# Kernel tuning notes

Measured on AMD Instinct MI355X. Metric: run time of the kernel, lower is better.

Reference implementation:

```python
import jax, jax.numpy as jnp
import numpy as np

DIM = 128
NUM_HEADS = 4
HEAD_DIM = DIM // NUM_HEADS
WS = 8            # window height/width
SHIFT = 4
N_CAND = 4        # candidates per spatial position
H_RES, W_RES = 64, 128
M = WS * WS       # tokens per window spatially
L = M * N_CAND    # window sequence length
NW = (H_RES // WS) * (W_RES // WS)
B = 1
B_ = NW * B
NEG_INF = -1e9  # finite stand-in for -inf; softmax result identical within fp tolerance


def _rel_position_index():
    ch = np.arange(WS); cw = np.arange(WS)
    coords = np.stack(np.meshgrid(ch, cw, indexing='ij')).reshape(2, -1)  # [2, M]
    rel = (coords[:, :, None] - coords[:, None, :]).transpose(1, 2, 0)    # [M, M, 2]
    rel = rel + np.array([WS - 1, WS - 1])
    rel[..., 0] *= 2 * WS - 1
    return rel.sum(-1).astype(np.int32)  # [M, M] in [0, (2WS-1)^2)


def _window_attn_mask():
    # block message passing between same spatial position's candidates (except self)
    idx = np.repeat(np.arange(M), N_CAND).astype(np.float64)  # [L]
    m = idx[:, None] - idx[None, :]
    mask = np.where(m == 0, NEG_INF, 0.0)
    mask[np.arange(L), np.arange(L)] = 0.0
    return mask  # [L, L]


def _shift_window_attn_mask():
    img = np.zeros((H_RES, W_RES))
    cnt = 0
    for hs in (slice(0, -WS), slice(-WS, -SHIFT), slice(-SHIFT, None)):
        for ws in (slice(0, -WS), slice(-WS, -SHIFT), slice(-SHIFT, None)):
            img[hs, ws] = cnt
            cnt += 1
    mw = img.reshape(H_RES // WS, WS, W_RES // WS, WS).transpose(0, 2, 1, 3).reshape(-1, M)  # [nW, M]
    am = mw[:, None, :] - mw[:, :, None]           # [nW, M, M]
    am = np.where(am != 0, NEG_INF, 0.0)
    am = np.repeat(np.repeat(am, N_CAND, axis=1), N_CAND, axis=2)  # [nW, L, L]
    return am + _window_attn_mask()[None]


def setup_inputs() -> dict:
    key = jax.random.key(0)
    ks = jax.random.split(key, 6)
    x = jax.random.normal(ks[0], (B_, L, DIM), dtype=jnp.float32)
    qkv_w = jax.random.normal(ks[1], (3 * DIM, DIM), dtype=jnp.float32) * 0.02
    qkv_b = jnp.zeros((3 * DIM,), dtype=jnp.float32)
    rpe_table = jax.random.normal(ks[2], ((2 * WS - 1) ** 2, 3 * DIM), dtype=jnp.float32) * 0.02
    proj_w = jax.random.normal(ks[3], (DIM, DIM), dtype=jnp.float32) * 0.02
    proj_b = jnp.zeros((DIM,), dtype=jnp.float32)
    attn_mask = jnp.asarray(_shift_window_attn_mask(), dtype=jnp.float32)
    rel_idx = jnp.asarray(_rel_position_index())
    return {"x": x, "qkv_w": qkv_w, "qkv_b": qkv_b, "rpe_table": rpe_table,
            "proj_w": proj_w, "proj_b": proj_b, "attn_mask": attn_mask, "rel_idx": rel_idx}


def reference(x, qkv_w, qkv_b, rpe_table, proj_w, proj_b, attn_mask, rel_idx):
    b_, l, _ = x.shape
    h, hd = NUM_HEADS, HEAD_DIM
    scale = hd ** -0.5
    # QKV projection -> [B_, h, L, hd] each
    qkv = (x @ qkv_w.T + qkv_b).reshape(b_, l, 3, h, hd).transpose(2, 0, 3, 1, 4)
    q, k, v = qkv[0], qkv[1], qkv[2]
    # relative-position encodings gathered per (i, j) pair, expanded over candidates
    m = rel_idx.shape[0]
    n = l // m
    rpe = rpe_table[rel_idx.reshape(-1)].reshape(m, m, h, 3 * hd)
    rpe = jnp.repeat(jnp.repeat(rpe, n, axis=0), n, axis=1)  # [L, L, h, 3*hd]
    q_rpe, k_rpe, v_rpe = jnp.split(rpe, 3, axis=-1)
    q = q * scale
    q_rpe = q_rpe * scale
    qk = jnp.einsum('bhic,bhjc->bhij', q, k)
    qr = jnp.einsum('bhic,ijhc->bhij', q, k_rpe)
    kr = jnp.einsum('bhjc,ijhc->bhij', k, q_rpe)
    attn = qk + qr + kr  # [B_, h, L, L]
    nw = attn_mask.shape[0]
    attn = attn.reshape(b_ // nw, nw, h, l, l) + attn_mask[None, :, None]
    attn = attn.reshape(b_, h, l, l)
    attn = jax.nn.softmax(attn.astype(jnp.float32), axis=-1).astype(x.dtype)
    out = jnp.einsum('bhij,bhjc->bhic', attn, v) + jnp.einsum('bhij,ijhc->bhic', attn, v_rpe)
    out = out.transpose(0, 2, 1, 3).reshape(b_, l, DIM)
    return out @ proj_w.T + proj_b
```

## Files before the change

### kernel.cpp

```cpp
#include <hip/hip_runtime.h>
#include <math.h>

constexpr int HD    = 32;
constexpr int LW    = 256;
constexpr int NWIN  = 128;
constexpr int ROWS  = NWIN * LW;
constexpr int QKVC  = 384;
constexpr float SCALE = 0.17677669529663687f;

__device__ inline float dot4(const float4 a, const float4 b) {
  return a.x * b.x + a.y * b.y + a.z * b.z + a.w * b.w;
}

__global__ __launch_bounds__(256) void rpe_gather_kernel(
    const float* __restrict__ tab, const int* __restrict__ rel_idx,
    float* __restrict__ out)
{
  int gid = blockIdx.x * 256 + threadIdx.x;
  int s   = gid % 96;
  int hp  = gid / 96;
  int p   = hp & 4095;
  int h   = hp >> 12;
  float v = tab[(size_t)rel_idx[p] * 384 + h * 96 + s];
  if (s < 32) v *= SCALE;
  out[gid] = v;
}

template <int N, int K>
__global__ __launch_bounds__(256) void gemm_nt_bias_v3(
    const float* __restrict__ A, const float* __restrict__ W,
    const float* __restrict__ bias, float* __restrict__ C)
{
  constexpr int BK  = 8;
  constexpr int NS  = K / BK;
  constexpr int LDP = 144;
  __shared__ float As[2][BK][LDP];
  __shared__ float Ws[2][BK][LDP];

  const int tid  = threadIdx.x;
  const int tx   = tid & 15;
  const int ty   = tid >> 4;
  const int srow = tid >> 1;
  const int skk  = (tid & 1) << 2;
  const int sphys = srow + ((srow >> 5) << 2);

  const float* Ag = A + ((size_t)blockIdx.x * 128 + srow) * K + skk;
  const float* Wg = W + ((size_t)blockIdx.y * 128 + srow) * K + skk;

  float4 ra = *(const float4*)(Ag);
  float4 rw = *(const float4*)(Wg);
  As[0][skk + 0][sphys] = ra.x; As[0][skk + 1][sphys] = ra.y;
  As[0][skk + 2][sphys] = ra.z; As[0][skk + 3][sphys] = ra.w;
  Ws[0][skk + 0][sphys] = rw.x; Ws[0][skk + 1][sphys] = rw.y;
  Ws[0][skk + 2][sphys] = rw.z; Ws[0][skk + 3][sphys] = rw.w;
  __syncthreads();

  const int mA = ty * 8; const int pA = mA + ((mA >> 5) << 2);
  const int mB = tx * 8; const int pB = mB + ((mB >> 5) << 2);

  float acc[8][8] = {};

  for (int s = 0; s < NS; ++s) {
    const int cur = s & 1;
    if (s + 1 < NS) {
      const int k0 = (s + 1) * BK;
      ra = *(const float4*)(Ag + k0);
      rw = *(const float4*)(Wg + k0);
    }
#pragma unroll
    for (int k = 0; k < BK; ++k) {
      float4 a0 = *(const float4*)&As[cur][k][pA];
      float4 a1 = *(const float4*)&As[cur][k][pA + 4];
      float4 b0 = *(const float4*)&Ws[cur][k][pB];
      float4 b1 = *(const float4*)&Ws[cur][k][pB + 4];
      float av[8] = {a0.x, a0.y, a0.z, a0.w, a1.x, a1.y, a1.z, a1.w};
      float bv[8] = {b0.x, b0.y, b0.z, b0.w, b1.x, b1.y, b1.z, b1.w};
#pragma unroll
      for (int i = 0; i < 8; ++i)
#pragma unroll
        for (int j = 0; j < 8; ++j)
          acc[i][j] += av[i] * bv[j];
    }
    if (s + 1 < NS) {
      const int nxt = (s + 1) & 1;
      As[nxt][skk + 0][sphys] = ra.x; As[nxt][skk + 1][sphys] = ra.y;
      As[nxt][skk + 2][sphys] = ra.z; As[nxt][skk + 3][sphys] = ra.w;
      Ws[nxt][skk + 0][sphys] = rw.x; Ws[nxt][skk + 1][sphys] = rw.y;
      Ws[nxt][skk + 2][sphys] = rw.z; Ws[nxt][skk + 3][sphys] = rw.w;
      __syncthreads();
    }
  }

  const int crow = blockIdx.x * 128 + ty * 8;
  const int ccol = blockIdx.y * 128 + tx * 8;
  float4 bb0 = *(const float4*)(bias + ccol);
  float4 bb1 = *(const float4*)(bias + ccol + 4);
#pragma unroll
  for (int i = 0; i < 8; ++i) {
    float4 r0, r1;
    r0.x = acc[i][0] + bb0.x; r0.y = acc[i][1] + bb0.y;
    r0.z = acc[i][2] + bb0.z; r0.w = acc[i][3] + bb0.w;
    r1.x = acc[i][4] + bb1.x; r1.y = acc[i][5] + bb1.y;
    r1.z = acc[i][6] + bb1.z; r1.w = acc[i][7] + bb1.w;
    *(float4*)(C + (size_t)(crow + i) * N + ccol)     = r0;
    *(float4*)(C + (size_t)(crow + i) * N + ccol + 4) = r1;
  }
}

__global__ __launch_bounds__(512) void attn_kernel(
    const float* __restrict__ qkv, const float* __restrict__ rpeg,
    const float* __restrict__ mask, float* __restrict__ out)
{
  __shared__ float ms[256 * 33];
  const int b = blockIdx.x;
  const int h = blockIdx.y;
  const int tid = threadIdx.x;
  const int row = tid & 255;
  const int jh  = __builtin_amdgcn_readfirstlane(tid >> 8);
  const size_t rowbase = (size_t)b * LW;

  const float* kvbase = qkv + rowbase * QKVC + 128 + h * HD;

  float4 q[8];
  {
    const float4* qr = (const float4*)(qkv + (rowbase + row) * QKVC + h * HD);
#pragma unroll
    for (int d = 0; d < 8; ++d) {
      float4 t = qr[d];
      q[d] = make_float4(t.x * SCALE, t.y * SCALE, t.z * SCALE, t.w * SCALE);
    }
  }
  const float4* rp4base =
      (const float4*)(rpeg + ((size_t)h * 4096 + (size_t)(row >> 2) * 64) * 96);
  const float* mrow = mask + ((size_t)b * LW + row) * LW;

  float4 acc[8];
#pragma unroll
  for (int d = 0; d < 8; ++d) acc[d] = make_float4(0.f, 0.f, 0.f, 0.f);
  float l_run = 0.f;
  const int jbase = jh << 5;

  for (int l = 0; l < 32; ++l) {
    const int j4 = jbase + l;
    const float4* rp = rp4base + j4 * 24;
    float4 uq[8];
    float c0 = 0.f;
#pragma unroll
    for (int d = 0; d < 8; ++d) {
      float4 sq = rp[d];
      float4 kr = rp[8 + d];
      uq[d] = make_float4(q[d].x + sq.x, q[d].y + sq.y,
                          q[d].z + sq.z, q[d].w + sq.w);
      c0 += dot4(q[d], kr);
    }
    float4 mv = *(const float4*)(mrow + j4 * 4);
    const float* kj0 = kvbase + (size_t)(j4 * 4) * QKVC;
    float s[4] = {mv.x + c0, mv.y + c0, mv.z + c0, mv.w + c0};
#pragma unroll
    for (int jc = 0; jc < 4; ++jc) {
      const float4* kj = (const float4*)(kj0 + jc * QKVC);
      float sa = 0.f;
#pragma unroll
      for (int d = 0; d < 8; ++d) sa += dot4(uq[d], kj[d]);
      s[jc] += sa;
    }
    float p[4];
    p[0] = __expf(s[0]); p[1] = __expf(s[1]);
    p[2] = __expf(s[2]); p[3] = __expf(s[3]);
    float pool = (p[0] + p[1]) + (p[2] + p[3]);
    l_run += pool;
#pragma unroll
    for (int jc = 0; jc < 4; ++jc) {
      const float4* vj = (const float4*)(kj0 + jc * QKVC + 128);
      float pj = p[jc];
#pragma unroll
      for (int d = 0; d < 8; ++d) {
        acc[d].x += pj * vj[d].x; acc[d].y += pj * vj[d].y;
        acc[d].z += pj * vj[d].z; acc[d].w += pj * vj[d].w;
      }
    }
#pragma unroll
    for (int d = 0; d < 8; ++d) {
      float4 vr = rp[16 + d];
      acc[d].x += pool * vr.x; acc[d].y += pool * vr.y;
      acc[d].z += pool * vr.z; acc[d].w += pool * vr.w;
    }
  }

  __syncthreads();
  if (jh == 1) {
    float* dst = &ms[row * 33];
#pragma unroll
    for (int d = 0; d < 8; ++d) {
      dst[d * 4 + 0] = acc[d].x; dst[d * 4 + 1] = acc[d].y;
      dst[d * 4 + 2] = acc[d].z; dst[d * 4 + 3] = acc[d].w;
    }
    dst[32] = l_run;
  }
  __syncthreads();
  if (jh == 0) {
    const float* src = &ms[row * 33];
    float inv = 1.f / (l_run + src[32]);
    float4* orow = (float4*)(out + (rowbase + row) * (4 * HD) + h * HD);
#pragma unroll
    for (int d = 0; d < 8; ++d) {
      float4 r;
      r.x = (acc[d].x + src[d * 4 + 0]) * inv;
      r.y = (acc[d].y + src[d * 4 + 1]) * inv;
      r.z = (acc[d].z + src[d * 4 + 2]) * inv;
      r.w = (acc[d].w + src[d * 4 + 3]) * inv;
      orow[d] = r;
    }
  }
}

extern "C" void kernel_launch(void* const* d_in, const int* in_sizes, int n_in,
                              void* d_out, int out_size, void* d_ws, size_t ws_size,
                              hipStream_t stream) {
  (void)in_sizes; (void)n_in; (void)out_size; (void)ws_size;
  const float* x         = (const float*)d_in[0];
  const float* qkv_w     = (const float*)d_in[1];
  const float* qkv_b     = (const float*)d_in[2];
  const float* rpe_table = (const float*)d_in[3];
  const float* proj_w    = (const float*)d_in[4];
  const float* proj_b    = (const float*)d_in[5];
  const float* attn_mask = (const float*)d_in[6];
  const int*   rel_idx   = (const int*)d_in[7];
  float* out = (float*)d_out;

  float* qkvbuf = (float*)d_ws;
  float* rpeg   = qkvbuf + (size_t)ROWS * QKVC;
  float* attnb  = rpeg + (size_t)4 * 4096 * 96;

  hipLaunchKernelGGL(rpe_gather_kernel, dim3(6144), dim3(256), 0, stream,
                     rpe_table, rel_idx, rpeg);
  hipLaunchKernelGGL((gemm_nt_bias_v3<QKVC, 128>), dim3(ROWS / 128, QKVC / 128),
                     dim3(256), 0, stream, x, qkv_w, qkv_b, qkvbuf);
  hipLaunchKernelGGL(attn_kernel, dim3(NWIN, 4), dim3(512), 0, stream,
                     qkvbuf, rpeg, attn_mask, attnb);
  hipLaunchKernelGGL((gemm_nt_bias_v3<128, 128>), dim3(ROWS / 128, 1),
                     dim3(256), 0, stream, attnb, proj_w, proj_b, out);
}
```

Measured before the change: 368.1 us.

## Use bf16 MFMA GEMMs for QKV and output projections

Replaces the fp32 FMA tiled GEMMs with bf16 MFMA 16x16x32 kernels. Adds cast kernels that convert x and both weight matrices to bf16. The attention kernel now writes its output in bf16 so it can feed the projection GEMM directly. This aims to cut GEMM compute time at the cost of extra cast passes and reduced precision.

```diff
diff --git a/kernel.cpp b/kernel.cpp
--- a/kernel.cpp
+++ b/kernel.cpp
@@ -8,8 +8,29 @@
 constexpr int QKVC  = 384;
 constexpr float SCALE = 0.17677669529663687f;
 
+typedef __attribute__((ext_vector_type(8))) short short8;
+typedef __attribute__((ext_vector_type(4))) float f32x4;
+union I4S8 { int4 i; short8 s; };
+
 __device__ inline float dot4(const float4 a, const float4 b) {
   return a.x * b.x + a.y * b.y + a.z * b.z + a.w * b.w;
+}
+
+__device__ inline unsigned short f2bf(float f) {
+  unsigned u = __float_as_uint(f);
+  unsigned r = (u + 0x7FFFu + ((u >> 16) & 1u)) >> 16;
+  return (unsigned short)r;
+}
+
+__global__ __launch_bounds__(256) void cast_x4_kernel(
+    const float* __restrict__ in, unsigned short* __restrict__ out, int n4)
+{
+  int i = blockIdx.x * 256 + threadIdx.x;
+  if (i >= n4) return;
+  float4 v = ((const float4*)in)[i];
+  ushort4 o;
+  o.x = f2bf(v.x); o.y = f2bf(v.y); o.z = f2bf(v.z); o.w = f2bf(v.w);
+  ((ushort4*)out)[i] = o;
 }
 
 __global__ __launch_bounds__(256) void rpe_gather_kernel(
@@ -26,90 +47,82 @@
   out[gid] = v;
 }
 
-template <int N, int K>
-__global__ __launch_bounds__(256) void gemm_nt_bias_v3(
-    const float* __restrict__ A, const float* __restrict__ W,
+template <int N>
+__global__ __launch_bounds__(256) void gemm_mfma_bt(
+    const unsigned short* __restrict__ A, const unsigned short* __restrict__ W,
     const float* __restrict__ bias, float* __restrict__ C)
 {
-  constexpr int BK  = 8;
-  constexpr int NS  = K / BK;
-  constexpr int LDP = 144;
-  __shared__ float As[2][BK][LDP];
-  __shared__ float Ws[2][BK][LDP];
-
+  constexpr int K   = 128;
+  constexpr int LDI = 28;
+  __shared__ int As[128 * LDI];
+  __shared__ int Bs[128 * LDI];
   const int tid  = threadIdx.x;
-  const int tx   = tid & 15;
-  const int ty   = tid >> 4;
-  const int srow = tid >> 1;
-  const int skk  = (tid & 1) << 2;
-  const int sphys = srow + ((srow >> 5) << 2);
-
-  const float* Ag = A + ((size_t)blockIdx.x * 128 + srow) * K + skk;
-  const float* Wg = W + ((size_t)blockIdx.y * 128 + srow) * K + skk;
-
-  float4 ra = *(const float4*)(Ag);
-  float4 rw = *(const float4*)(Wg);
-  As[0][skk + 0][sphys] = ra.x; As[0][skk + 1][sphys] = ra.y;
-  As[0][skk + 2][sphys] = ra.z; As[0][skk + 3][sphys] = ra.w;
-  Ws[0][skk + 0][sphys] = rw.x; Ws[0][skk + 1][sphys] = rw.y;
-  Ws[0][skk + 2][sphys] = rw.z; Ws[0][skk + 3][sphys] = rw.w;
-  __syncthreads();
-
-  const int mA = ty * 8; const int pA = mA + ((mA >> 5) << 2);
-  const int mB = tx * 8; const int pB = mB + ((mB >> 5) << 2);
-
-  float acc[8][8] = {};
-
-  for (int s = 0; s < NS; ++s) {
-    const int cur = s & 1;
-    if (s + 1 < NS) {
-      const int k0 = (s + 1) * BK;
-      ra = *(const float4*)(Ag + k0);
-      rw = *(const float4*)(Wg + k0);
-    }
-#pragma unroll
-    for (int k = 0; k < BK; ++k) {
-      float4 a0 = *(const float4*)&As[cur][k][pA];
-      float4 a1 = *(const float4*)&As[cur][k][pA + 4];
-      float4 b0 = *(const float4*)&Ws[cur][k][pB];
-      float4 b1 = *(const float4*)&Ws[cur][k][pB + 4];
-      float av[8] = {a0.x, a0.y, a0.z, a0.w, a1.x, a1.y, a1.z, a1.w};
-      float bv[8] = {b0.x, b0.y, b0.z, b0.w, b1.x, b1.y, b1.z, b1.w};
-#pragma unroll
-      for (int i = 0; i < 8; ++i)
-#pragma unroll
-        for (int j = 0; j < 8; ++j)
-          acc[i][j] += av[i] * bv[j];
-    }
-    if (s + 1 < NS) {
-      const int nxt = (s + 1) & 1;
-      As[nxt][skk + 0][sphys] = ra.x; As[nxt][skk + 1][sphys] = ra.y;
-      As[nxt][skk + 2][sphys] = ra.z; As[nxt][skk + 3][sphys] = ra.w;
-      Ws[nxt][skk + 0][sphys] = rw.x; Ws[nxt][skk + 1][sphys] = rw.y;
-      Ws[nxt][skk + 2][sphys] = rw.z; Ws[nxt][skk + 3][sphys] = rw.w;
-      __syncthreads();
-    }
-  }
-
-  const int crow = blockIdx.x * 128 + ty * 8;
-  const int ccol = blockIdx.y * 128 + tx * 8;
-  float4 bb0 = *(const float4*)(bias + ccol);
-  float4 bb1 = *(const float4*)(bias + ccol + 4);
-#pragma unroll
-  for (int i = 0; i < 8; ++i) {
-    float4 r0, r1;
-    r0.x = acc[i][0] + bb0.x; r0.y = acc[i][1] + bb0.y;
-    r0.z = acc[i][2] + bb0.z; r0.w = acc[i][3] + bb0.w;
-    r1.x = acc[i][4] + bb1.x; r1.y = acc[i][5] + bb1.y;
-    r1.z = acc[i][6] + bb1.z; r1.w = acc[i][7] + bb1.w;
-    *(float4*)(C + (size_t)(crow + i) * N + ccol)     = r0;
-    *(float4*)(C + (size_t)(crow + i) * N + ccol + 4) = r1;
+  const int wave = tid >> 6;
+  const int lane = tid & 63;
+  const int lm   = lane & 15;
+  const int q    = lane >> 4;
+  const int m0   = blockIdx.x * 128;
+  const int n0   = blockIdx.y * 128;
+
+  const int* Ag = (const int*)(A + (size_t)m0 * K);
+  const int* Wg = (const int*)(W + (size_t)n0 * K);
+
+  const int srow = tid >> 2;
+  const int sk4  = (tid & 3) * 4;
+
+  f32x4 acc[2][8] = {};
+
+  for (int ks = 0; ks < 4; ++ks) {
+    const int goff = ks * 16 + sk4;
+    int4 a0 = *(const int4*)(Ag + (size_t)srow * 64 + goff);
+    int4 a1 = *(const int4*)(Ag + (size_t)(srow + 64) * 64 + goff);
+    int4 w0 = *(const int4*)(Wg + (size_t)srow * 64 + goff);
+    int4 w1 = *(const int4*)(Wg + (size_t)(srow + 64) * 64 + goff);
+    *(int4*)&As[srow * LDI + sk4]        = a0;
+    *(int4*)&As[(srow + 64) * LDI + sk4] = a1;
+    *(int4*)&Bs[srow * LDI + sk4]        = w0;
+    *(int4*)&Bs[(srow + 64) * LDI + sk4] = w1;
+    __syncthreads();
+
+    short8 af[2], bf[8];
+#pragma unroll
+    for (int t = 0; t < 2; ++t) {
+      const int m = (wave * 2 + t) * 16 + lm;
+      I4S8 u; u.i = *(const int4*)&As[m * LDI + q * 4];
+      af[t] = u.s;
+    }
+#pragma unroll
+    for (int nt = 0; nt < 8; ++nt) {
+      const int n = nt * 16 + lm;
+      I4S8 u; u.i = *(const int4*)&Bs[n * LDI + q * 4];
+      bf[nt] = u.s;
+    }
+#pragma unroll
+    for (int t = 0; t < 2; ++t)
+#pragma unroll
+      for (int nt = 0; nt < 8; ++nt)
+        acc[t][nt] = __builtin_amdgcn_mfma_f32_16x16x32_bf16(
+            af[t], bf[nt], acc[t][nt], 0, 0, 0);
+    __syncthreads();
+  }
+
+#pragma unroll
+  for (int t = 0; t < 2; ++t) {
+    const int mrow = m0 + (wave * 2 + t) * 16 + q * 4;
+#pragma unroll
+    for (int nt = 0; nt < 8; ++nt) {
+      const int col = n0 + nt * 16 + lm;
+      const float bb = bias[col];
+#pragma unroll
+      for (int r = 0; r < 4; ++r)
+        C[(size_t)(mrow + r) * N + col] = acc[t][nt][r] + bb;
+    }
   }
 }
 
 __global__ __launch_bounds__(512) void attn_kernel(
     const float* __restrict__ qkv, const float* __restrict__ rpeg,
-    const float* __restrict__ mask, float* __restrict__ out)
+    const float* __restrict__ mask, unsigned short* __restrict__ out)
 {
   __shared__ float ms[256 * 33];
   const int b = blockIdx.x;
@@ -201,15 +214,15 @@
   if (jh == 0) {
     const float* src = &ms[row * 33];
     float inv = 1.f / (l_run + src[32]);
-    float4* orow = (float4*)(out + (rowbase + row) * (4 * HD) + h * HD);
-#pragma unroll
-    for (int d = 0; d < 8; ++d) {
-      float4 r;
-      r.x = (acc[d].x + src[d * 4 + 0]) * inv;
-      r.y = (acc[d].y + src[d * 4 + 1]) * inv;
-      r.z = (acc[d].z + src[d * 4 + 2]) * inv;
-      r.w = (acc[d].w + src[d * 4 + 3]) * inv;
-      orow[d] = r;
+    unsigned short* orow = out + (rowbase + row) * 128 + h * HD;
+#pragma unroll
+    for (int d = 0; d < 8; ++d) {
+      ushort4 r;
+      r.x = f2bf((acc[d].x + src[d * 4 + 0]) * inv);
+      r.y = f2bf((acc[d].y + src[d * 4 + 1]) * inv);
+      r.z = f2bf((acc[d].z + src[d * 4 + 2]) * inv);
+      r.w = f2bf((acc[d].w + src[d * 4 + 3]) * inv);
+      *(ushort4*)(orow + d * 4) = r;
     }
   }
 }
@@ -230,14 +243,24 @@
 
   float* qkvbuf = (float*)d_ws;
   float* rpeg   = qkvbuf + (size_t)ROWS * QKVC;
-  float* attnb  = rpeg + (size_t)4 * 4096 * 96;
-
+  unsigned short* xbf    = (unsigned short*)(rpeg + (size_t)4 * 4096 * 96);
+  unsigned short* qkvwbf = xbf + (size_t)ROWS * 128;
+  unsigned short* projwbf= qkvwbf + (size_t)QKVC * 128;
+  unsigned short* attnbf = projwbf + (size_t)128 * 128;
+
+  hipLaunchKernelGGL(cast_x4_kernel, dim3(ROWS * 128 / 4 / 256), dim3(256), 0,
+                     stream, x, xbf, ROWS * 128 / 4);
+  hipLaunchKernelGGL(cast_x4_kernel, dim3(48), dim3(256), 0, stream,
+                     qkv_w, qkvwbf, QKVC * 128 / 4);
+  hipLaunchKernelGGL(cast_x4_kernel, dim3(16), dim3(256), 0, stream,
+                     proj_w, projwbf, 128 * 128 / 4);
   hipLaunchKernelGGL(rpe_gather_kernel, dim3(6144), dim3(256), 0, stream,
                      rpe_table, rel_idx, rpeg);
-  hipLaunchKernelGGL((gemm_nt_bias_v3<QKVC, 128>), dim3(ROWS / 128, QKVC / 128),
-                     dim3(256), 0, stream, x, qkv_w, qkv_b, qkvbuf);
+
+  hipLaunchKernelGGL((gemm_mfma_bt<QKVC>), dim3(ROWS / 128, QKVC / 128),
+                     dim3(256), 0, stream, xbf, qkvwbf, qkv_b, qkvbuf);
   hipLaunchKernelGGL(attn_kernel, dim3(NWIN, 4), dim3(512), 0, stream,
-                     qkvbuf, rpeg, attn_mask, attnb);
-  hipLaunchKernelGGL((gemm_nt_bias_v3<128, 128>), dim3(ROWS / 128, 1),
-                     dim3(256), 0, stream, attnb, proj_w, proj_b, out);
-}
+                     qkvbuf, rpeg, attn_mask, attnbf);
+  hipLaunchKernelGGL((gemm_mfma_bt<128>), dim3(ROWS / 128, 1),
+                     dim3(256), 0, stream, attnbf, projwbf, proj_b, out);
+}
```

New measurement: 325.9 us. -11.4%, faster.
